# Kernel tuning notes

Measured on AMD Instinct MI355X. Metric: run time of the kernel, lower is better.

## Reference

```python
import jax, jax.numpy as jnp
import numpy as np

N = 50000
E = 800000
G = 16  # graphs in batch
NEG_SLOPE = 0.2


def gatv2_layer(x, src, dst, Wl, bl, Wr, br, att, bias, concat):
    # PyG GATv2Conv: x_j = lin_l(x)[src], x_i = lin_r(x)[dst]
    H, C = att.shape
    n = x.shape[0]
    xl = (x @ Wl + bl).reshape(n, H, C)  # source transform
    xr = (x @ Wr + br).reshape(n, H, C)  # target transform
    e = jax.nn.leaky_relu(xl[src] + xr[dst], NEG_SLOPE)  # [E,H,C]
    score = jnp.einsum('ehc,hc->eh', e, att)             # [E,H]
    # segment softmax over incoming edges of each dst node
    smax = jax.ops.segment_max(score, dst, num_segments=n)   # [n,H]
    ex = jnp.exp(score - smax[dst])
    denom = jax.ops.segment_sum(ex, dst, num_segments=n)
    alpha = ex / (denom[dst] + 1e-16)                        # [E,H]
    out = jax.ops.segment_sum(alpha[:, :, None] * xl[src], dst, num_segments=n)  # [n,H,C]
    if concat:
        return out.reshape(n, H * C) + bias
    return out.mean(axis=1) + bias


def setup_inputs() -> dict:
    key = jax.random.key(0)
    ks = jax.random.split(key, 20)
    x = jax.random.normal(ks[0], (N, 8), dtype=jnp.float32)
    edge_index = jax.random.randint(ks[1], (2, E), 0, N, dtype=jnp.int64)
    batch = jnp.sort(jax.random.randint(ks[2], (N,), 0, G, dtype=jnp.int64))

    def glorot(k, shape):
        lim = np.sqrt(6.0 / (shape[0] + shape[1]))
        return jax.random.uniform(k, shape, jnp.float32, -lim, lim)

    params = dict(
        Wl1=glorot(ks[3], (8, 128)), bl1=jnp.zeros((128,), jnp.float32),
        Wr1=glorot(ks[4], (8, 128)), br1=jnp.zeros((128,), jnp.float32),
        att1=glorot(ks[5], (2, 64)), b1=jnp.zeros((128,), jnp.float32),
        Wl2=glorot(ks[6], (128, 128)), bl2=jnp.zeros((128,), jnp.float32),
        Wr2=glorot(ks[7], (128, 128)), br2=jnp.zeros((128,), jnp.float32),
        att2=glorot(ks[8], (2, 64)), b2=jnp.zeros((128,), jnp.float32),
        Wl3=glorot(ks[9], (128, 32)), bl3=jnp.zeros((32,), jnp.float32),
        Wr3=glorot(ks[10], (128, 32)), br3=jnp.zeros((32,), jnp.float32),
        att3=glorot(ks[11], (1, 32)), b3=jnp.zeros((32,), jnp.float32),
    )
    return dict(x=x, edge_index=edge_index, batch=batch, **params)


def reference(x, edge_index, batch,
              Wl1, bl1, Wr1, br1, att1, b1,
              Wl2, bl2, Wr2, br2, att2, b2,
              Wl3, bl3, Wr3, br3, att3, b3):
    n = x.shape[0]
    loops = jnp.arange(n, dtype=edge_index.dtype)
    src = jnp.concatenate([edge_index[0], loops])  # add_self_loops=True (PyG default)
    dst = jnp.concatenate([edge_index[1], loops])

    h = gatv2_layer(x, src, dst, Wl1, bl1, Wr1, br1, att1, b1, concat=True)
    h = jax.nn.elu(h)
    # dropout(p=0.5) is identity in eval mode
    h = gatv2_layer(h, src, dst, Wl2, bl2, Wr2, br2, att2, b2, concat=True)
    h = jax.nn.elu(h)
    h = gatv2_layer(h, src, dst, Wl3, bl3, Wr3, br3, att3, b3, concat=False)
    h = jax.nn.elu(h)  # [n,32]

    counts = jax.ops.segment_sum(jnp.ones((n,), h.dtype), batch, num_segments=G)
    pooled_mean = jax.ops.segment_sum(h, batch, num_segments=G) / counts[:, None]
    pooled_max = jax.ops.segment_max(h, batch, num_segments=G)
    return jnp.concatenate([pooled_mean, pooled_max], axis=1)  # [G,64]
```

## Files before the change

kernel.cpp:

```cpp
#include <hip/hip_runtime.h>
#include <hip/hip_bf16.h>
#include <math.h>


__device__ __forceinline__ float lrelu(float x) { return x > 0.f ? x : 0.2f * x; }
__device__ __forceinline__ float elu1(float x) { return x > 0.f ? x : expm1f(x); }

__device__ __forceinline__ unsigned f2ord(float x) {
    unsigned b = __float_as_uint(x);
    return (b & 0x80000000u) ? ~b : (b | 0x80000000u);
}
__device__ __forceinline__ float ord2f(unsigned u) {
    unsigned b = (u & 0x80000000u) ? (u & 0x7FFFFFFFu) : ~u;
    return __uint_as_float(b);
}

__global__ void k_zero_i32(int* __restrict__ p, int n) {
    int i = blockIdx.x * blockDim.x + threadIdx.x;
    if (i < n) p[i] = 0;
}

__global__ void k_hist(const int* __restrict__ ei, int E, int N, int* __restrict__ deg) {
    int e = blockIdx.x * blockDim.x + threadIdx.x;
    int Etot = E + N;
    if (e >= Etot) return;
    int d = (e < E) ? ei[E + e] : (e - E);
    atomicAdd(&deg[d], 1);
}

__global__ void __launch_bounds__(1024) k_scan(const int* __restrict__ deg, int n,
                                               int* __restrict__ row_off, int* __restrict__ cursor) {
    __shared__ int wsum[16];
    __shared__ int sbase;
    int tid = threadIdx.x;
    int lane = tid & 63, w = tid >> 6;
    if (tid == 0) sbase = 0;
    __syncthreads();
    for (int start = 0; start < n; start += 1024) {
        int i = start + tid;
        int v = (i < n) ? deg[i] : 0;
        int s = v;
        #pragma unroll
        for (int d = 1; d < 64; d <<= 1) {
            int t = __shfl_up(s, d, 64);
            if (lane >= d) s += t;
        }
        if (lane == 63) wsum[w] = s;
        __syncthreads();
        int wbase = 0;
        for (int k = 0; k < w; k++) wbase += wsum[k];
        int excl = sbase + wbase + (s - v);
        if (i < n) { row_off[i] = excl; cursor[i] = excl; }
        __syncthreads();
        if (tid == 1023) sbase = excl + v;
        __syncthreads();
    }
    if (tid == 0) row_off[n] = sbase;
}

__global__ void k_scatter(const int* __restrict__ ei, int E, int N,
                          int* __restrict__ cursor,
                          int* __restrict__ csr_src) {
    int e = blockIdx.x * blockDim.x + threadIdx.x;
    int Etot = E + N;
    if (e >= Etot) return;
    int s, d;
    if (e < E) { s = ei[e]; d = ei[E + e]; } else { s = e - E; d = e - E; }
    int p = atomicAdd(&cursor[d], 1);
    csr_src[p] = s;
}

template <int K, int MH>
__global__ void k_linear2(const float* __restrict__ x, int N,
                          const float* __restrict__ Wl, const float* __restrict__ bl,
                          const float* __restrict__ Wr, const float* __restrict__ br,
                          float* __restrict__ xl, float* __restrict__ xr) {
    constexpr int NCG = MH / 2;
    __shared__ float xs[32 * K];
    int tid = threadIdx.x;
    int node0 = blockIdx.x * 32;
    for (int idx = tid * 4; idx < 32 * K; idx += NCG * 4 * 4) {
        int node = node0 + idx / K;
        float4 v = make_float4(0.f, 0.f, 0.f, 0.f);
        if (node < N) v = *(const float4*)(x + (size_t)node0 * K + idx);
        *(float4*)(xs + idx) = v;
    }
    __syncthreads();

    int cg = tid % NCG;
    int ng = tid / NCG;
    bool rightSide = cg >= (MH / 4);
    int c = (rightSide ? cg - MH / 4 : cg) * 4;
    const float* W  = rightSide ? Wr : Wl;
    const float* bb = rightSide ? br : bl;
    float* out      = rightSide ? xr : xl;

    float acc[8][4];
    #pragma unroll
    for (int i = 0; i < 8; i++)
        #pragma unroll
        for (int j = 0; j < 4; j++) acc[i][j] = 0.f;

    const float* xrow = xs + ng * 8 * K;
    for (int k0 = 0; k0 < K; k0 += 4) {
        float4 wv[4];
        #pragma unroll
        for (int kk = 0; kk < 4; kk++)
            wv[kk] = *(const float4*)(W + (size_t)(k0 + kk) * MH + c);
        #pragma unroll
        for (int i = 0; i < 8; i++) {
            float4 xv = *(const float4*)(xrow + i * K + k0);
            float xvk[4] = {xv.x, xv.y, xv.z, xv.w};
            #pragma unroll
            for (int kk = 0; kk < 4; kk++) {
                acc[i][0] += xvk[kk] * wv[kk].x;
                acc[i][1] += xvk[kk] * wv[kk].y;
                acc[i][2] += xvk[kk] * wv[kk].z;
                acc[i][3] += xvk[kk] * wv[kk].w;
            }
        }
    }
    float4 bv = *(const float4*)(bb + c);
    #pragma unroll
    for (int i = 0; i < 8; i++) {
        int node = node0 + ng * 8 + i;
        if (node < N) {
            float4 o = make_float4(acc[i][0] + bv.x, acc[i][1] + bv.y,
                                   acc[i][2] + bv.z, acc[i][3] + bv.w);
            *(float4*)(out + (size_t)node * MH + c) = o;
        }
    }
}

template <int CPL>
__device__ __forceinline__ void loadrow(const float* __restrict__ p, float* v) {
    if constexpr (CPL == 8) {
        float4 a = ((const float4*)p)[0];
        float4 b = ((const float4*)p)[1];
        v[0] = a.x; v[1] = a.y; v[2] = a.z; v[3] = a.w;
        v[4] = b.x; v[5] = b.y; v[6] = b.z; v[7] = b.w;
    } else {
        float2 a = ((const float2*)p)[0];
        v[0] = a.x; v[1] = a.y;
    }
}

template <int HC, int C>
__global__ void k_fused(const int* __restrict__ row_off, const int* __restrict__ csr_src,
                        const float* __restrict__ xl, const float* __restrict__ xr,
                        const float* __restrict__ att, const float* __restrict__ bias,
                        float* __restrict__ hout, int N) {
    constexpr int CPL = HC / 16;
    constexpr int GROUP = (16 * C) / HC;
    int wid = (blockIdx.x * blockDim.x + threadIdx.x) >> 6;
    int lane = threadIdx.x & 63;
    if (wid >= N) return;
    int slot = lane >> 4;
    int j = lane & 15;
    int c0 = j * CPL;

    int p0 = row_off[wid], p1 = row_off[wid + 1];

    float xrv[CPL], attv[CPL];
    loadrow<CPL>(xr + (size_t)wid * HC + c0, xrv);
    loadrow<CPL>(att + c0, attv);

    float m = -INFINITY, den = 0.f;
    float acc[CPL];
    #pragma unroll
    for (int q = 0; q < CPL; q++) acc[q] = 0.f;

    int p = p0 + slot;
    int s = (p < p1) ? csr_src[p] : 0;
    while (p < p1) {
        int pn = p + 4;
        int sn = (pn < p1) ? csr_src[pn] : 0;
        float xlv[CPL];
        loadrow<CPL>(xl + (size_t)s * HC + c0, xlv);
        float part = 0.f;
        #pragma unroll
        for (int q = 0; q < CPL; q++) part += lrelu(xlv[q] + xrv[q]) * attv[q];
        #pragma unroll
        for (int msk = 1; msk < GROUP; msk <<= 1) part += __shfl_xor(part, msk, 64);
        float mnew = fmaxf(m, part);
        float corr = __expf(m - mnew);
        float ex = __expf(part - mnew);
        den = den * corr + ex;
        #pragma unroll
        for (int q = 0; q < CPL; q++) acc[q] = acc[q] * corr + ex * xlv[q];
        m = mnew;
        p = pn; s = sn;
    }
    float mAll = fmaxf(m, __shfl_xor(m, 16, 64));
    mAll = fmaxf(mAll, __shfl_xor(mAll, 32, 64));
    float scale = __expf(m - mAll);
    float dtot = den * scale;
    dtot += __shfl_xor(dtot, 16, 64);
    dtot += __shfl_xor(dtot, 32, 64);
    #pragma unroll
    for (int q = 0; q < CPL; q++) {
        float a = acc[q] * scale;
        a += __shfl_xor(a, 16, 64);
        a += __shfl_xor(a, 32, 64);
        acc[q] = a;
    }
    if (slot == 0) {
        float inv = 1.0f / (dtot + 1e-16f);
        #pragma unroll
        for (int q = 0; q < CPL; q++) {
            float v = acc[q] * inv + bias[c0 + q];
            hout[(size_t)wid * HC + c0 + q] = elu1(v);
        }
    }
}

__global__ void __launch_bounds__(256) k_pool_partial(
        const float* __restrict__ h, const int* __restrict__ batch, int N, int G,
        float* __restrict__ gsum, unsigned* __restrict__ gmax) {
    __shared__ float lsum[512];
    __shared__ unsigned lmax[512];
    int tid = threadIdx.x;
    for (int i = tid; i < G * 32; i += 256) { lsum[i] = 0.f; lmax[i] = 0u; }
    __syncthreads();
    int chunk = (N + gridDim.x - 1) / gridDim.x;
    int start = blockIdx.x * chunk;
    int end = min(N, start + chunk);
    int col = tid & 31, row = tid >> 5;
    int gc = -1; float ps = 0.f; unsigned pm = 0u;
    for (int i = start + row; i < end; i += 8) {
        int g = batch[i];
        if (g != gc) {
            if (gc >= 0) { atomicAdd(&lsum[gc * 32 + col], ps); atomicMax(&lmax[gc * 32 + col], pm); }
            gc = g; ps = 0.f; pm = 0u;
        }
        float v = h[(size_t)i * 32 + col];
        ps += v; pm = max(pm, f2ord(v));
    }
    if (gc >= 0) { atomicAdd(&lsum[gc * 32 + col], ps); atomicMax(&lmax[gc * 32 + col], pm); }
    __syncthreads();
    for (int i = tid; i < G * 32; i += 256) {
        if (lmax[i]) {
            atomicAdd(&gsum[i], lsum[i]);
            atomicMax(&gmax[i], lmax[i]);
        }
    }
}

__global__ void k_pool_final(const float* __restrict__ gsum, const unsigned* __restrict__ gmax,
                             const int* __restrict__ batch, int N, float* __restrict__ out) {
    int g = blockIdx.x;
    int t = threadIdx.x;
    __shared__ int s_cnt;
    if (t == 0) {
        int lo = 0, hi = N;
        while (lo < hi) { int m = (lo + hi) >> 1; if (batch[m] < g) lo = m + 1; else hi = m; }
        int a = lo;
        lo = a; hi = N;
        while (lo < hi) { int m = (lo + hi) >> 1; if (batch[m] < g + 1) lo = m + 1; else hi = m; }
        s_cnt = lo - a;
    }
    __syncthreads();
    if (t < 32) {
        out[g * 64 + t] = gsum[g * 32 + t] / (float)max(s_cnt, 1);
    } else {
        out[g * 64 + t] = ord2f(gmax[g * 32 + (t - 32)]);
    }
}

extern "C" void kernel_launch(void* const* d_in, const int* in_sizes, int n_in,
                              void* d_out, int out_size, void* d_ws, size_t ws_size,
                              hipStream_t stream) {
    const float* x      = (const float*)d_in[0];
    const int*   ei     = (const int*)d_in[1];
    const int*   batch  = (const int*)d_in[2];
    const float* Wl1 = (const float*)d_in[3],  *bl1 = (const float*)d_in[4];
    const float* Wr1 = (const float*)d_in[5],  *br1 = (const float*)d_in[6];
    const float* att1= (const float*)d_in[7],  *b1  = (const float*)d_in[8];
    const float* Wl2 = (const float*)d_in[9],  *bl2 = (const float*)d_in[10];
    const float* Wr2 = (const float*)d_in[11], *br2 = (const float*)d_in[12];
    const float* att2= (const float*)d_in[13], *b2  = (const float*)d_in[14];
    const float* Wl3 = (const float*)d_in[15], *bl3 = (const float*)d_in[16];
    const float* Wr3 = (const float*)d_in[17], *br3 = (const float*)d_in[18];
    const float* att3= (const float*)d_in[19], *b3  = (const float*)d_in[20];

    int N = in_sizes[0] / 8;
    int E = in_sizes[1] / 2;
    int G = out_size / 64;
    int Etot = E + N;

    char* w = (char*)d_ws;
    auto carve = [&](size_t bytes) {
        void* p = (void*)w;
        w += (bytes + 255) & ~(size_t)255;
        return p;
    };
    int*      deg     = (int*)carve((size_t)N * 4);
    int*      row_off = (int*)carve((size_t)(N + 1) * 4);
    int*      cursor  = (int*)carve((size_t)N * 4);
    int*      csr_src = (int*)carve((size_t)Etot * 4);
    float*    gsum    = (float*)carve((size_t)G * 32 * 4);
    unsigned* gmax    = (unsigned*)carve((size_t)G * 32 * 4);
    float*    bufA    = (float*)carve((size_t)N * 128 * 4);
    float*    bufB    = (float*)carve((size_t)N * 128 * 4);
    float*    bufC    = (float*)carve((size_t)N * 128 * 4);
    (void)ws_size; (void)n_in;

    k_zero_i32<<<(N + 255) / 256, 256, 0, stream>>>(deg, N);
    k_zero_i32<<<(2 * G * 32 + 255) / 256, 256, 0, stream>>>((int*)gsum, 2 * G * 32);
    k_hist<<<(Etot + 255) / 256, 256, 0, stream>>>(ei, E, N, deg);
    k_scan<<<1, 1024, 0, stream>>>(deg, N, row_off, cursor);
    k_scatter<<<(Etot + 255) / 256, 256, 0, stream>>>(ei, E, N, cursor, csr_src);

    int grdLin = (N + 31) / 32;
    int grdFused = (N + 3) / 4;

    k_linear2<8, 128><<<grdLin, 256, 0, stream>>>(x, N, Wl1, bl1, Wr1, br1, bufA, bufB);
    k_fused<128, 64><<<grdFused, 256, 0, stream>>>(row_off, csr_src, bufA, bufB, att1, b1, bufC, N);

    k_linear2<128, 128><<<grdLin, 256, 0, stream>>>(bufC, N, Wl2, bl2, Wr2, br2, bufA, bufB);
    k_fused<128, 64><<<grdFused, 256, 0, stream>>>(row_off, csr_src, bufA, bufB, att2, b2, bufC, N);

    k_linear2<128, 32><<<grdLin, 64, 0, stream>>>(bufC, N, Wl3, bl3, Wr3, br3, bufA, bufB);
    k_fused<32, 32><<<grdFused, 256, 0, stream>>>(row_off, csr_src, bufA, bufB, att3, b3, bufC, N);

    k_pool_partial<<<256, 256, 0, stream>>>(bufC, batch, N, G, gsum, gmax);
    k_pool_final<<<G, 64, 0, stream>>>(gsum, gmax, batch, N, (float*)d_out);
}
```

Before: 538.5 us.

## Fuse layer-1 linear transforms into attention by aggregating raw 8-dim inputs

```diff
diff --git a/kernel.cpp b/kernel.cpp
--- a/kernel.cpp
+++ b/kernel.cpp
@@ -68,6 +68,118 @@
     if (e < E) { s = ei[e]; d = ei[E + e]; } else { s = e - E; d = e - E; }
     int p = atomicAdd(&cursor[d], 1);
     csr_src[p] = s;
+}
+
+__global__ void __launch_bounds__(256) k_fused1(
+        const int* __restrict__ row_off, const int* __restrict__ csr_src,
+        const float* __restrict__ x,
+        const float* __restrict__ Wl, const float* __restrict__ bl,
+        const float* __restrict__ Wr, const float* __restrict__ br,
+        const float* __restrict__ att,
+        const float* __restrict__ bias,
+        float* __restrict__ hout, int N) {
+    int wid = (blockIdx.x * blockDim.x + threadIdx.x) >> 6;
+    int lane = threadIdx.x & 63;
+    if (wid >= N) return;
+    int slot = lane >> 4;
+    int j = lane & 15;
+    int c0 = j * 8;
+
+    float wl[8][8];
+    #pragma unroll
+    for (int k = 0; k < 8; k++) {
+        float4 a = *(const float4*)(Wl + k * 128 + c0);
+        float4 b = *(const float4*)(Wl + k * 128 + c0 + 4);
+        wl[k][0] = a.x; wl[k][1] = a.y; wl[k][2] = a.z; wl[k][3] = a.w;
+        wl[k][4] = b.x; wl[k][5] = b.y; wl[k][6] = b.z; wl[k][7] = b.w;
+    }
+    float blv[8], attv[8];
+    {
+        float4 a = *(const float4*)(bl + c0), b = *(const float4*)(bl + c0 + 4);
+        blv[0] = a.x; blv[1] = a.y; blv[2] = a.z; blv[3] = a.w;
+        blv[4] = b.x; blv[5] = b.y; blv[6] = b.z; blv[7] = b.w;
+        float4 c = *(const float4*)(att + c0), d = *(const float4*)(att + c0 + 4);
+        attv[0] = c.x; attv[1] = c.y; attv[2] = c.z; attv[3] = c.w;
+        attv[4] = d.x; attv[5] = d.y; attv[6] = d.z; attv[7] = d.w;
+    }
+    float xrv[8];
+    {
+        float4 d0 = *(const float4*)(x + (size_t)wid * 8);
+        float4 d1 = *(const float4*)(x + (size_t)wid * 8 + 4);
+        float xd[8] = {d0.x, d0.y, d0.z, d0.w, d1.x, d1.y, d1.z, d1.w};
+        float4 r0 = *(const float4*)(br + c0), r1 = *(const float4*)(br + c0 + 4);
+        xrv[0] = r0.x; xrv[1] = r0.y; xrv[2] = r0.z; xrv[3] = r0.w;
+        xrv[4] = r1.x; xrv[5] = r1.y; xrv[6] = r1.z; xrv[7] = r1.w;
+        #pragma unroll
+        for (int k = 0; k < 8; k++) {
+            float4 a = *(const float4*)(Wr + k * 128 + c0);
+            float4 b = *(const float4*)(Wr + k * 128 + c0 + 4);
+            xrv[0] = fmaf(xd[k], a.x, xrv[0]); xrv[1] = fmaf(xd[k], a.y, xrv[1]);
+            xrv[2] = fmaf(xd[k], a.z, xrv[2]); xrv[3] = fmaf(xd[k], a.w, xrv[3]);
+            xrv[4] = fmaf(xd[k], b.x, xrv[4]); xrv[5] = fmaf(xd[k], b.y, xrv[5]);
+            xrv[6] = fmaf(xd[k], b.z, xrv[6]); xrv[7] = fmaf(xd[k], b.w, xrv[7]);
+        }
+    }
+
+    int p0 = row_off[wid], p1 = row_off[wid + 1];
+    float m = -INFINITY, den = 0.f;
+    float acc[8];
+    #pragma unroll
+    for (int k = 0; k < 8; k++) acc[k] = 0.f;
+
+    int p = p0 + slot;
+    int s = (p < p1) ? csr_src[p] : 0;
+    while (p < p1) {
+        int pn = p + 4;
+        int sn = (pn < p1) ? csr_src[pn] : 0;
+        float4 a = *(const float4*)(x + (size_t)s * 8);
+        float4 b = *(const float4*)(x + (size_t)s * 8 + 4);
+        float xs_[8] = {a.x, a.y, a.z, a.w, b.x, b.y, b.z, b.w};
+        float sc = 0.f;
+        #pragma unroll
+        for (int q = 0; q < 8; q++) {
+            float v = blv[q];
+            #pragma unroll
+            for (int k = 0; k < 8; k++) v = fmaf(xs_[k], wl[k][q], v);
+            float t = v + xrv[q];
+            sc = fmaf(fmaxf(t, 0.2f * t), attv[q], sc);
+        }
+        sc += __shfl_xor(sc, 1, 64);
+        sc += __shfl_xor(sc, 2, 64);
+        sc += __shfl_xor(sc, 4, 64);
+        float mnew = fmaxf(m, sc);
+        float corr = __expf(m - mnew);
+        float ex = __expf(sc - mnew);
+        den = den * corr + ex;
+        #pragma unroll
+        for (int k = 0; k < 8; k++) acc[k] = fmaf(ex, xs_[k], acc[k] * corr);
+        m = mnew;
+        p = pn; s = sn;
+    }
+    float mAll = fmaxf(m, __shfl_xor(m, 16, 64));
+    mAll = fmaxf(mAll, __shfl_xor(mAll, 32, 64));
+    float scale = __expf(m - mAll);
+    float dtot = den * scale;
+    dtot += __shfl_xor(dtot, 16, 64);
+    dtot += __shfl_xor(dtot, 32, 64);
+    #pragma unroll
+    for (int k = 0; k < 8; k++) {
+        float a2 = acc[k] * scale;
+        a2 += __shfl_xor(a2, 16, 64);
+        a2 += __shfl_xor(a2, 32, 64);
+        acc[k] = a2;
+    }
+    if (slot == 0) {
+        float inv = 1.0f / (dtot + 1e-16f);
+        #pragma unroll
+        for (int q = 0; q < 8; q++) {
+            float v = blv[q];
+            #pragma unroll
+            for (int k = 0; k < 8; k++) v = fmaf(acc[k] * inv, wl[k][q], v);
+            v += bias[c0 + q];
+            hout[(size_t)wid * 128 + c0 + q] = elu1(v);
+        }
+    }
 }
 
 template <int K, int MH>
@@ -128,6 +240,65 @@
             float4 o = make_float4(acc[i][0] + bv.x, acc[i][1] + bv.y,
                                    acc[i][2] + bv.z, acc[i][3] + bv.w);
             *(float4*)(out + (size_t)node * MH + c) = o;
+        }
+    }
+}
+
+__global__ void __launch_bounds__(256) k_linear3(
+        const float* __restrict__ x, int N,
+        const float* __restrict__ Wl, const float* __restrict__ bl,
+        const float* __restrict__ Wr, const float* __restrict__ br,
+        float* __restrict__ xl, float* __restrict__ xr) {
+    __shared__ float xs[32 * 128];
+    int tid = threadIdx.x;
+    int node0 = blockIdx.x * 32;
+    for (int idx = tid * 4; idx < 32 * 128; idx += 256 * 4) {
+        int node = node0 + idx / 128;
+        float4 v = make_float4(0.f, 0.f, 0.f, 0.f);
+        if (node < N) v = *(const float4*)(x + (size_t)node0 * 128 + idx);
+        *(float4*)(xs + idx) = v;
+    }
+    __syncthreads();
+    int cg = tid & 15, ng = tid >> 4;
+    bool rightSide = cg >= 8;
+    int c = (rightSide ? cg - 8 : cg) * 4;
+    const float* W  = rightSide ? Wr : Wl;
+    const float* bb = rightSide ? br : bl;
+    float* out      = rightSide ? xr : xl;
+
+    float acc[2][4];
+    #pragma unroll
+    for (int i = 0; i < 2; i++)
+        #pragma unroll
+        for (int j = 0; j < 4; j++) acc[i][j] = 0.f;
+
+    const float* xrow = xs + ng * 2 * 128;
+    for (int k0 = 0; k0 < 128; k0 += 4) {
+        float4 wv[4];
+        #pragma unroll
+        for (int kk = 0; kk < 4; kk++)
+            wv[kk] = *(const float4*)(W + (size_t)(k0 + kk) * 32 + c);
+        #pragma unroll
+        for (int i = 0; i < 2; i++) {
+            float4 xv = *(const float4*)(xrow + i * 128 + k0);
+            float xvk[4] = {xv.x, xv.y, xv.z, xv.w};
+            #pragma unroll
+            for (int kk = 0; kk < 4; kk++) {
+                acc[i][0] += xvk[kk] * wv[kk].x;
+                acc[i][1] += xvk[kk] * wv[kk].y;
+                acc[i][2] += xvk[kk] * wv[kk].z;
+                acc[i][3] += xvk[kk] * wv[kk].w;
+            }
+        }
+    }
+    float4 bv = *(const float4*)(bb + c);
+    #pragma unroll
+    for (int i = 0; i < 2; i++) {
+        int node = node0 + ng * 2 + i;
+        if (node < N) {
+            float4 o = make_float4(acc[i][0] + bv.x, acc[i][1] + bv.y,
+                                   acc[i][2] + bv.z, acc[i][3] + bv.w);
+            *(float4*)(out + (size_t)node * 32 + c) = o;
         }
     }
 }
@@ -314,13 +485,13 @@
     int grdLin = (N + 31) / 32;
     int grdFused = (N + 3) / 4;
 
-    k_linear2<8, 128><<<grdLin, 256, 0, stream>>>(x, N, Wl1, bl1, Wr1, br1, bufA, bufB);
-    k_fused<128, 64><<<grdFused, 256, 0, stream>>>(row_off, csr_src, bufA, bufB, att1, b1, bufC, N);
+    k_fused1<<<grdFused, 256, 0, stream>>>(row_off, csr_src, x,
+                                           Wl1, bl1, Wr1, br1, att1, b1, bufC, N);
 
     k_linear2<128, 128><<<grdLin, 256, 0, stream>>>(bufC, N, Wl2, bl2, Wr2, br2, bufA, bufB);
     k_fused<128, 64><<<grdFused, 256, 0, stream>>>(row_off, csr_src, bufA, bufB, att2, b2, bufC, N);
 
-    k_linear2<128, 32><<<grdLin, 64, 0, stream>>>(bufC, N, Wl3, bl3, Wr3, br3, bufA, bufB);
+    k_linear3<<<grdLin, 256, 0, stream>>>(bufC, N, Wl3, bl3, Wr3, br3, bufA, bufB);
     k_fused<32, 32><<<grdFused, 256, 0, stream>>>(row_off, csr_src, bufA, bufB, att3, b3, bufC, N);
 
     k_pool_partial<<<256, 256, 0, stream>>>(bufC, batch, N, G, gsum, gmax);
```

Result: slower. 641.7 us (+19.2%).
